# Optimization experiments

Hardware: AMD Instinct MI355X
Metric: run time of the kernel (lower is better)

The kernel has to match this reference:

```python
import jax, jax.numpy as jnp
import numpy as np

B, S, D = 2, 2048, 1024
H, DA, DL = 8, 64, 64   # heads, attention_dim, linear_dim
L = 2                    # num_blocks


def _layernorm(x, w, b, eps):
    mu = jnp.mean(x, axis=-1, keepdims=True)
    var = jnp.mean(jnp.square(x - mu), axis=-1, keepdims=True)
    return (x - mu) * jax.lax.rsqrt(var + eps) * w + b


def _norm_no_affine(x, eps):
    mu = jnp.mean(x, axis=-1, keepdims=True)
    var = jnp.mean(jnp.square(x - mu), axis=-1, keepdims=True)
    return (x - mu) * jax.lax.rsqrt(var + eps)


def setup_inputs() -> dict:
    key = jax.random.key(0)
    ks = jax.random.split(key, 8)
    x = jax.random.normal(ks[0], (B, S, D), dtype=jnp.float32)
    # causal visibility mask: True = visible
    attn_mask = jnp.tril(jnp.ones((S, S), dtype=bool))[None].repeat(B, axis=0)
    proj_dim = DL * 2 * H + DA * 2 * H  # 2048
    uvqk = jax.random.normal(ks[1], (L, D, proj_dim), dtype=jnp.float32) * 0.02
    o_w = jax.random.normal(ks[2], (L, D, DL * H), dtype=jnp.float32) * 0.02  # torch [out,in]
    o_b = jnp.zeros((L, D), dtype=jnp.float32)
    ln_w = jnp.ones((L, D), dtype=jnp.float32)
    ln_b = jnp.zeros((L, D), dtype=jnp.float32)
    last_ln_w = jnp.ones((D,), dtype=jnp.float32)
    last_ln_b = jnp.zeros((D,), dtype=jnp.float32)
    return {"x": x, "attn_mask": attn_mask, "uvqk": uvqk, "o_w": o_w,
            "o_b": o_b, "ln_w": ln_w, "ln_b": ln_b,
            "last_ln_w": last_ln_w, "last_ln_b": last_ln_b}


def reference(x, attn_mask, uvqk, o_w, o_b, ln_w, ln_b, last_ln_w, last_ln_b):
    seq_len = x.shape[1]
    m = attn_mask[:, None, :, :]  # [B,1,S,S]
    for i in range(L):
        h = _layernorm(x, ln_w[i], ln_b[i], 1e-6)                 # [B,S,D]
        proj = jax.nn.silu(jnp.einsum('bsd,de->bse', h, uvqk[i]))  # [B,S,2*(DL+DA)*H]
        u, v, q, k = jnp.split(proj, [DL * H, 2 * DL * H, 2 * DL * H + DA * H], axis=-1)
        q = q.reshape(B, seq_len, H, DA).transpose(0, 2, 1, 3)   # [B,H,S,DA]
        kk = k.reshape(B, seq_len, H, DA).transpose(0, 2, 1, 3)
        vv = v.reshape(B, seq_len, H, DL).transpose(0, 2, 1, 3)  # [B,H,S,DL]
        uu = u.reshape(B, seq_len, H, DL).transpose(0, 2, 1, 3)
        scores = jnp.einsum('bhsd,bhtd->bhst', q, kk)            # [B,H,S,S]
        scores = jnp.where(m, jax.nn.silu(scores) / seq_len, 0.0)
        out = jnp.einsum('bhst,bhtd->bhsd', scores, vv)          # [B,H,S,DL]
        out = _norm_no_affine(out, 1e-6)
        u_dot = (uu * out).transpose(0, 2, 1, 3).reshape(B, seq_len, DL * H)
        x = x + jnp.einsum('bsf,df->bsd', u_dot, o_w[i]) + o_b[i]
    return _layernorm(x, last_ln_w, last_ln_b, 1e-8)
```

## Files before the change

kernel.cpp:

```cpp
#include <hip/hip_runtime.h>

#define B_ 2
#define S_ 2048
#define D_ 1024
#define H_ 8
#define L_ 2
#define P_ 2048
#define F_ 512
#define R_ (B_*S_)

typedef unsigned short u16;
typedef unsigned int u32;
typedef __bf16 bf16;
typedef bf16 bf16x8 __attribute__((ext_vector_type(8)));
typedef short short8 __attribute__((ext_vector_type(8)));
typedef float v4f __attribute__((ext_vector_type(4)));

__device__ __forceinline__ float silu_fast(float x){
  float e = __expf(-x);
  return x * __builtin_amdgcn_rcpf(1.0f + e);
}
__device__ __forceinline__ float bf2f(u16 u){
  union { u32 i; float f; } x; x.i = ((u32)u) << 16; return x.f;
}
__device__ __forceinline__ u16 f2bfu(float f){
  union { float f; u32 i; } x; x.f = f;
  u32 r = x.i + 0x7fff + ((x.i >> 16) & 1);
  return (u16)(r >> 16);
}
__device__ __forceinline__ void gload16(const u16* g, u16* l){
  __builtin_amdgcn_global_load_lds(
      (const __attribute__((address_space(1))) void*)g,
      (__attribute__((address_space(3))) void*)l, 16, 0, 0);
}

__global__ __launch_bounds__(256) void cvt_kernel(const float* __restrict__ x, float* __restrict__ xf){
  int i = (blockIdx.x * 256 + threadIdx.x) * 4;
  *(float4*)(xf + i) = *(const float4*)(x + i);
}

__global__ __launch_bounds__(256) void cvt_bf16_kernel(const float* __restrict__ src, u16* __restrict__ dst){
  int i = (blockIdx.x * 256 + threadIdx.x) * 4;
  float4 v = *(const float4*)(src + i);
  ushort4 o; o.x = f2bfu(v.x); o.y = f2bfu(v.y); o.z = f2bfu(v.z); o.w = f2bfu(v.w);
  *(ushort4*)(dst + i) = o;
}

__global__ __launch_bounds__(256) void cvt_uvqkT_kernel(const float* __restrict__ uvqk, u16* __restrict__ ot){
  __shared__ float t[32][33];
  int l = blockIdx.z;
  int p0 = blockIdx.x * 32, d0 = blockIdx.y * 32;
  int tx = threadIdx.x & 31, ty = threadIdx.x >> 5;
  const float* src = uvqk + ((size_t)l * D_ + d0) * P_ + p0;
  #pragma unroll
  for (int s = 0; s < 4; s++)
    t[ty + s*8][tx] = src[(size_t)(ty + s*8) * P_ + tx];
  __syncthreads();
  u16* dst = ot + ((size_t)l * P_ + p0) * D_ + d0;
  #pragma unroll
  for (int s = 0; s < 4; s++)
    dst[(size_t)(ty + s*8) * D_ + tx] = f2bfu(t[tx][ty + s*8]);
}

__global__ __launch_bounds__(256) void kvpack_kernel(const u16* __restrict__ projh,
    u16* __restrict__ kpack, u16* __restrict__ vpack){
  __shared__ u16 tls[64*72];
  int t = blockIdx.x, t0 = t * 64;
  int bh = blockIdx.y;
  int b = bh >> 3, hh = bh & 7;
  int tid = threadIdx.x;
  const size_t bS = (size_t)b * S_;
  const int voff = F_ + hh*64, koff = 3*F_ + hh*64;
  {
    int row = tid >> 2, c16 = (tid & 3) * 16;
    const u16* sp = projh + (bS + t0 + row) * P_ + voff + c16;
    short8 a = *(const short8*)sp;
    short8 bq = *(const short8*)(sp + 8);
    *(short8*)&tls[row*72 + c16] = a;
    *(short8*)&tls[row*72 + c16 + 8] = bq;
  }
  __syncthreads();
  size_t obase = ((size_t)(bh*32 + t) * 8) * 512;
  #pragma unroll
  for (int pass = 0; pass < 2; pass++){
    int id = tid + pass * 256;
    int c = id >> 6, lane = id & 63;
    int quad = lane >> 4, l15 = lane & 15;
    int cns = c >> 1, ckst = c & 1;
    const u16* kp = projh + (bS + t0 + cns*16 + l15) * P_ + koff + ckst*32 + quad*8;
    *(short8*)(kpack + obase + (size_t)c*512 + lane*8) = *(const short8*)kp;
    short8 vv;
    #pragma unroll
    for (int j = 0; j < 8; j++)
      vv[j] = (short)tls[(ckst*32 + quad*8 + j)*72 + cns*16 + l15];
    *(short8*)(vpack + obase + (size_t)c*512 + lane*8) = vv;
  }
}

__global__ __launch_bounds__(256) void ln_kernel(const float* __restrict__ xf,
    const float* __restrict__ w, const float* __restrict__ b,
    void* __restrict__ outp, float eps, int out_bf16){
  int row = blockIdx.x, tid = threadIdx.x;
  const float* xr = xf + (size_t)row * D_;
  float4 v = *(const float4*)(xr + tid * 4);
  float s  = v.x + v.y + v.z + v.w;
  float sq = v.x*v.x + v.y*v.y + v.z*v.z + v.w*v.w;
  #pragma unroll
  for (int off = 32; off; off >>= 1){ s += __shfl_down(s, off); sq += __shfl_down(sq, off); }
  __shared__ float red[8];
  __shared__ float stats[2];
  int wid = tid >> 6;
  if ((tid & 63) == 0){ red[wid] = s; red[4 + wid] = sq; }
  __syncthreads();
  if (tid == 0){
    float S1 = red[0] + red[1] + red[2] + red[3];
    float S2 = red[4] + red[5] + red[6] + red[7];
    float mu = S1 * (1.0f / D_);
    float var = S2 * (1.0f / D_) - mu * mu;
    stats[0] = mu; stats[1] = rsqrtf(var + eps);
  }
  __syncthreads();
  float mu = stats[0], rs = stats[1];
  int i = tid * 4;
  float4 wv = *(const float4*)(w + i);
  float4 bv = *(const float4*)(b + i);
  float o0 = (v.x - mu) * rs * wv.x + bv.x;
  float o1 = (v.y - mu) * rs * wv.y + bv.y;
  float o2 = (v.z - mu) * rs * wv.z + bv.z;
  float o3 = (v.w - mu) * rs * wv.w + bv.w;
  if (out_bf16){
    ushort4 o; o.x = f2bfu(o0); o.y = f2bfu(o1); o.z = f2bfu(o2); o.w = f2bfu(o3);
    *(ushort4*)((u16*)outp + (size_t)row * D_ + i) = o;
  } else {
    *(float4*)((float*)outp + (size_t)row * D_ + i) = make_float4(o0, o1, o2, o3);
  }
}

template<int KDIM>
__device__ __forceinline__ void gemm_mfma_core(const u16* __restrict__ A,
    const u16* __restrict__ Bt, u16* As, u16* Bs, int m0, int n0, v4f acc[4][4]){
  int tid = threadIdx.x;
  int w = tid >> 6, lane = tid & 63;
  int wm = w >> 1, wn = w & 1, quad = lane >> 4, l15 = lane & 15;
  int srow = lane >> 2, skoct = (lane & 3) * 8;
  for (int kt = 0; kt < KDIM; kt += 32){
    __syncthreads();
    #pragma unroll
    for (int s = 0; s < 2; s++){
      int g = w * 2 + s;
      gload16(A  + (size_t)(m0 + g*16 + srow) * KDIM + kt + skoct, As + g*512);
      gload16(Bt + (size_t)(n0 + g*16 + srow) * KDIM + kt + skoct, Bs + g*512);
    }
    __syncthreads();
    short8 af[4], bfr[4];
    #pragma unroll
    for (int i = 0; i < 4; i++)
      af[i] = *(const short8*)&As[(wm*64 + i*16 + l15)*32 + quad*8];
    #pragma unroll
    for (int j = 0; j < 4; j++)
      bfr[j] = *(const short8*)&Bs[(wn*64 + j*16 + l15)*32 + quad*8];
    #pragma unroll
    for (int i = 0; i < 4; i++)
      #pragma unroll
      for (int j = 0; j < 4; j++)
        acc[i][j] = __builtin_amdgcn_mfma_f32_16x16x32_bf16(
            __builtin_bit_cast(bf16x8, af[i]), __builtin_bit_cast(bf16x8, bfr[j]),
            acc[i][j], 0, 0, 0);
  }
}

__global__ __launch_bounds__(256) void gemm_silu_mfma(const u16* __restrict__ A,
    const u16* __restrict__ Bt, u16* __restrict__ C){
  __shared__ u16 As[128*32], Bs[128*32];
  v4f acc[4][4];
  #pragma unroll
  for (int i = 0; i < 4; i++)
    #pragma unroll
    for (int j = 0; j < 4; j++) acc[i][j] = (v4f){0.f,0.f,0.f,0.f};
  int m0 = blockIdx.y * 128, n0 = blockIdx.x * 128;
  gemm_mfma_core<D_>(A, Bt, As, Bs, m0, n0, acc);
  int tid = threadIdx.x, w = tid >> 6, lane = tid & 63;
  int wm = w >> 1, wn = w & 1, quad = lane >> 4, l15 = lane & 15;
  #pragma unroll
  for (int i = 0; i < 4; i++)
    #pragma unroll
    for (int r = 0; r < 4; r++){
      int m = m0 + wm*64 + i*16 + quad*4 + r;
      u16* cp = C + (size_t)m * P_ + n0 + wn*64 + l15;
      #pragma unroll
      for (int j = 0; j < 4; j++)
        cp[j*16] = f2bfu(silu_fast(acc[i][j][r]));
    }
}

__global__ __launch_bounds__(256) void gemm_add_mfma(const u16* __restrict__ A,
    const u16* __restrict__ Bt, const float* __restrict__ bias, float* __restrict__ X){
  __shared__ u16 As[128*32], Bs[128*32];
  v4f acc[4][4];
  #pragma unroll
  for (int i = 0; i < 4; i++)
    #pragma unroll
    for (int j = 0; j < 4; j++) acc[i][j] = (v4f){0.f,0.f,0.f,0.f};
  int m0 = blockIdx.y * 128, n0 = blockIdx.x * 128;
  gemm_mfma_core<F_>(A, Bt, As, Bs, m0, n0, acc);
  int tid = threadIdx.x, w = tid >> 6, lane = tid & 63;
  int wm = w >> 1, wn = w & 1, quad = lane >> 4, l15 = lane & 15;
  float bj[4];
  #pragma unroll
  for (int j = 0; j < 4; j++) bj[j] = bias[n0 + wn*64 + j*16 + l15];
  #pragma unroll
  for (int i = 0; i < 4; i++)
    #pragma unroll
    for (int r = 0; r < 4; r++){
      int m = m0 + wm*64 + i*16 + quad*4 + r;
      float* xp = X + (size_t)m * D_ + n0 + wn*64 + l15;
      #pragma unroll
      for (int j = 0; j < 4; j++)
        xp[j*16] += acc[i][j][r] + bj[j];
    }
}

__global__ __launch_bounds__(256) void attn_kernel(const u16* __restrict__ projh,
                                                   const u16* __restrict__ kpack,
                                                   const u16* __restrict__ vpack,
                                                   u16* __restrict__ opart){
  __shared__ u16 ks[8*512];
  __shared__ u16 vs[8*512];
  __shared__ u16 Ps[64*72];
  int qt = 15 - (int)blockIdx.x;
  int z  = blockIdx.z;
  int ttop = 2*qt + 1;
  int bh = blockIdx.y;
  int b = bh >> 3, hh = bh & 7;
  int tid = threadIdx.x;
  int w = tid >> 6, lane = tid & 63, quad = lane >> 4, l15 = lane & 15;
  int s0 = qt * 128;
  const size_t bS = (size_t)b * S_;
  const int qoff = 2*F_ + hh*64;

  bf16x8 aq[2][2];
  #pragma unroll
  for (int qh = 0; qh < 2; qh++){
    const u16* qp = projh + (bS + s0 + qh*64 + w*16 + l15) * P_ + qoff + quad*8;
    aq[qh][0] = __builtin_bit_cast(bf16x8, *(const short8*)qp);
    aq[qh][1] = __builtin_bit_cast(bf16x8, *(const short8*)(qp + 32));
  }

  v4f oacc[2][4];
  #pragma unroll
  for (int qh = 0; qh < 2; qh++)
    #pragma unroll
    for (int i = 0; i < 4; i++) oacc[qh][i] = (v4f){0.f, 0.f, 0.f, 0.f};

  for (int t = z; t <= ttop; t += 2){
    size_t pbase = ((size_t)(bh*32 + t) * 8) * 512;
    __syncthreads();
    #pragma unroll
    for (int cc = 0; cc < 2; cc++){
      int c = w + cc*4;
      gload16(kpack + pbase + (size_t)c*512 + lane*8, ks + c*512);
      gload16(vpack + pbase + (size_t)c*512 + lane*8, vs + c*512);
    }
    __syncthreads();

    short8 vf[4][2];
    #pragma unroll
    for (int ds = 0; ds < 4; ds++)
      #pragma unroll
      for (int kst = 0; kst < 2; kst++)
        vf[ds][kst] = *(const short8*)&vs[(ds*2+kst)*512 + lane*8];

    int t0 = t * 64;
    #pragma unroll
    for (int qh = 0; qh < 2; qh++){
      int dtile = 2*qt + qh;
      if (t > dtile) continue;
      v4f sacc[4];
      #pragma unroll
      for (int i = 0; i < 4; i++) sacc[i] = (v4f){0.f, 0.f, 0.f, 0.f};
      #pragma unroll
      for (int ns = 0; ns < 4; ns++){
        bf16x8 bk0 = __builtin_bit_cast(bf16x8, *(const short8*)&ks[(ns*2+0)*512 + lane*8]);
        bf16x8 bk1 = __builtin_bit_cast(bf16x8, *(const short8*)&ks[(ns*2+1)*512 + lane*8]);
        sacc[ns] = __builtin_amdgcn_mfma_f32_16x16x32_bf16(aq[qh][0], bk0, sacc[ns], 0, 0, 0);
        sacc[ns] = __builtin_amdgcn_mfma_f32_16x16x32_bf16(aq[qh][1], bk1, sacc[ns], 0, 0, 0);
      }

      bool diag = (t == dtile);
      #pragma unroll
      for (int ns = 0; ns < 4; ns++){
        #pragma unroll
        for (int r = 0; r < 4; r++){
          int rl = w*16 + quad*4 + r;
          int cl = ns*16 + l15;
          float p = silu_fast(sacc[ns][r]) * (1.0f / S_);
          if (diag && cl > rl) p = 0.0f;
          Ps[rl*72 + cl] = f2bfu(p);
        }
      }
      #pragma unroll
      for (int kst = 0; kst < 2; kst++){
        short8 aps = *(const short8*)&Ps[(w*16 + l15)*72 + kst*32 + quad*8];
        bf16x8 ap = __builtin_bit_cast(bf16x8, aps);
        #pragma unroll
        for (int ds = 0; ds < 4; ds++)
          oacc[qh][ds] = __builtin_amdgcn_mfma_f32_16x16x32_bf16(
              ap, __builtin_bit_cast(bf16x8, vf[ds][kst]), oacc[qh][ds], 0, 0, 0);
      }
    }
  }

  u16* ob = opart + (size_t)z * ((size_t)R_ * F_);
  #pragma unroll
  for (int qh = 0; qh < 2; qh++){
    #pragma unroll
    for (int r = 0; r < 4; r++){
      int sg = s0 + qh*64 + w*16 + quad*4 + r;
      u16* op = ob + (bS + sg) * (size_t)F_ + hh*64 + l15;
      #pragma unroll
      for (int ds = 0; ds < 4; ds++)
        op[ds*16] = f2bfu(oacc[qh][ds][r]);
    }
  }
}

__global__ __launch_bounds__(256) void norm_gate_kernel(const u16* __restrict__ opart,
    const u16* __restrict__ projh, u16* __restrict__ udot){
  int w = threadIdx.x >> 6, lane = threadIdx.x & 63;
  int sg = blockIdx.x * 4 + w;
  int hh = lane >> 3, seg = lane & 7;
  size_t off = (size_t)sg * F_ + hh*64 + seg*8;
  short8 a0 = *(const short8*)(opart + off);
  short8 a1 = *(const short8*)(opart + (size_t)R_ * F_ + off);
  float e[8];
  float s = 0.f, sq = 0.f;
  #pragma unroll
  for (int i = 0; i < 8; i++){
    e[i] = bf2f((u16)a0[i]) + bf2f((u16)a1[i]);
    s += e[i]; sq += e[i]*e[i];
  }
  #pragma unroll
  for (int m = 1; m < 8; m <<= 1){
    s  += __shfl_xor(s, m, 64);
    sq += __shfl_xor(sq, m, 64);
  }
  float mu = s * (1.0f/64.0f);
  float var = sq * (1.0f/64.0f) - mu*mu;
  float rs = rsqrtf(var + 1e-6f);
  const u16* up = projh + (size_t)sg * P_ + hh*64 + seg*8;
  short8 uv = *(const short8*)up;
  short8 ov;
  #pragma unroll
  for (int i = 0; i < 8; i++)
    ov[i] = (short)f2bfu((e[i] - mu) * rs * bf2f((u16)uv[i]));
  *(short8*)(udot + off) = ov;
}

extern "C" void kernel_launch(void* const* d_in, const int* in_sizes, int n_in,
                              void* d_out, int out_size, void* d_ws, size_t ws_size,
                              hipStream_t stream){
  (void)in_sizes; (void)n_in; (void)out_size; (void)ws_size;
  const float* x     = (const float*)d_in[0];
  const float* uvqk  = (const float*)d_in[2];
  const float* o_w   = (const float*)d_in[3];
  const float* o_b   = (const float*)d_in[4];
  const float* ln_w  = (const float*)d_in[5];
  const float* ln_b  = (const float*)d_in[6];
  const float* lln_w = (const float*)d_in[7];
  const float* lln_b = (const float*)d_in[8];
  float* out = (float*)d_out;

  char* ws = (char*)d_ws;
  float* xf    = (float*)ws;
  u16*   h     = (u16*)(ws + (16u<<20));
  u16*   kpack = h;
  u16*   vpack = (u16*)(ws + (20u<<20));
  u16*   udot  = (u16*)(ws + (24u<<20));
  u16*   projh = (u16*)(ws + (28u<<20));
  u16*   uvqkT = (u16*)(ws + (44u<<20));
  u16*   owh   = (u16*)(ws + (52u<<20));
  u16*   opart = (u16*)(ws + (54u<<20));

  cvt_kernel<<<R_ * D_ / 1024, 256, 0, stream>>>(x, xf);
  cvt_uvqkT_kernel<<<dim3(P_/32, D_/32, L_), 256, 0, stream>>>(uvqk, uvqkT);
  cvt_bf16_kernel<<<L_ * D_ * F_ / 1024, 256, 0, stream>>>(o_w, owh);
  for (int l = 0; l < L_; l++){
    ln_kernel<<<R_, 256, 0, stream>>>(xf, ln_w + l * D_, ln_b + l * D_, h, 1e-6f, 1);
    gemm_silu_mfma<<<dim3(P_/128, R_/128), 256, 0, stream>>>(
        h, uvqkT + (size_t)l * P_ * D_, projh);
    kvpack_kernel<<<dim3(S_/64, B_*H_), 256, 0, stream>>>(projh, kpack, vpack);
    attn_kernel<<<dim3(S_/128, B_*H_, 2), 256, 0, stream>>>(projh, kpack, vpack, opart);
    norm_gate_kernel<<<R_/4, 256, 0, stream>>>(opart, projh, udot);
    gemm_add_mfma<<<dim3(D_/128, R_/128), 256, 0, stream>>>(
        udot, owh + (size_t)l * D_ * F_, o_b + l * D_, xf);
  }
  ln_kernel<<<R_, 256, 0, stream>>>(xf, lln_w, lln_b, out, 1e-8f, 0);
}
```

Baseline: 325.6 us.

## Double-buffer LDS tiles in GEMM and attention kernels to overlap loads

Both MFMA GEMM cores and the attention kernel now keep two LDS buffers. The next K-slice or K/V tile is prefetched into the other buffer while MFMAs run on the current one, with a single barrier at the end of each iteration instead of two. The goal is to hide global-to-LDS load latency behind compute. In exchange, LDS use doubles, which may lower occupancy, and correctness relies on the barrier also waiting for the outstanding loads.

```diff
diff --git a/kernel.cpp b/kernel.cpp
--- a/kernel.cpp
+++ b/kernel.cpp
@@ -143,22 +143,28 @@
   int w = tid >> 6, lane = tid & 63;
   int wm = w >> 1, wn = w & 1, quad = lane >> 4, l15 = lane & 15;
   int srow = lane >> 2, skoct = (lane & 3) * 8;
-  for (int kt = 0; kt < KDIM; kt += 32){
-    __syncthreads();
+  auto stage = [&](int buf, int kt){
     #pragma unroll
     for (int s = 0; s < 2; s++){
       int g = w * 2 + s;
-      gload16(A  + (size_t)(m0 + g*16 + srow) * KDIM + kt + skoct, As + g*512);
-      gload16(Bt + (size_t)(n0 + g*16 + srow) * KDIM + kt + skoct, Bs + g*512);
-    }
-    __syncthreads();
+      gload16(A  + (size_t)(m0 + g*16 + srow) * KDIM + kt + skoct, As + buf*4096 + g*512);
+      gload16(Bt + (size_t)(n0 + g*16 + srow) * KDIM + kt + skoct, Bs + buf*4096 + g*512);
+    }
+  };
+  stage(0, 0);
+  __syncthreads();
+  int cur = 0;
+  for (int kt = 0; kt < KDIM; kt += 32){
+    if (kt + 32 < KDIM) stage(cur ^ 1, kt + 32);
+    const u16* asb = As + cur*4096;
+    const u16* bsb = Bs + cur*4096;
     short8 af[4], bfr[4];
     #pragma unroll
     for (int i = 0; i < 4; i++)
-      af[i] = *(const short8*)&As[(wm*64 + i*16 + l15)*32 + quad*8];
+      af[i] = *(const short8*)&asb[(wm*64 + i*16 + l15)*32 + quad*8];
     #pragma unroll
     for (int j = 0; j < 4; j++)
-      bfr[j] = *(const short8*)&Bs[(wn*64 + j*16 + l15)*32 + quad*8];
+      bfr[j] = *(const short8*)&bsb[(wn*64 + j*16 + l15)*32 + quad*8];
     #pragma unroll
     for (int i = 0; i < 4; i++)
       #pragma unroll
@@ -166,12 +172,14 @@
         acc[i][j] = __builtin_amdgcn_mfma_f32_16x16x32_bf16(
             __builtin_bit_cast(bf16x8, af[i]), __builtin_bit_cast(bf16x8, bfr[j]),
             acc[i][j], 0, 0, 0);
+    __syncthreads();
+    cur ^= 1;
   }
 }
 
 __global__ __launch_bounds__(256) void gemm_silu_mfma(const u16* __restrict__ A,
     const u16* __restrict__ Bt, u16* __restrict__ C){
-  __shared__ u16 As[128*32], Bs[128*32];
+  __shared__ u16 As[2*128*32], Bs[2*128*32];
   v4f acc[4][4];
   #pragma unroll
   for (int i = 0; i < 4; i++)
@@ -195,7 +203,7 @@
 
 __global__ __launch_bounds__(256) void gemm_add_mfma(const u16* __restrict__ A,
     const u16* __restrict__ Bt, const float* __restrict__ bias, float* __restrict__ X){
-  __shared__ u16 As[128*32], Bs[128*32];
+  __shared__ u16 As[2*128*32], Bs[2*128*32];
   v4f acc[4][4];
   #pragma unroll
   for (int i = 0; i < 4; i++)
@@ -224,8 +232,8 @@
                                                    const u16* __restrict__ kpack,
                                                    const u16* __restrict__ vpack,
                                                    u16* __restrict__ opart){
-  __shared__ u16 ks[8*512];
-  __shared__ u16 vs[8*512];
+  __shared__ u16 ks[2*8*512];
+  __shared__ u16 vs[2*8*512];
   __shared__ u16 Ps[64*72];
   int qt = 15 - (int)blockIdx.x;
   int z  = blockIdx.z;
@@ -252,25 +260,32 @@
     #pragma unroll
     for (int i = 0; i < 4; i++) oacc[qh][i] = (v4f){0.f, 0.f, 0.f, 0.f};
 
-  for (int t = z; t <= ttop; t += 2){
+  auto stage = [&](int buf, int t){
     size_t pbase = ((size_t)(bh*32 + t) * 8) * 512;
-    __syncthreads();
     #pragma unroll
     for (int cc = 0; cc < 2; cc++){
       int c = w + cc*4;
-      gload16(kpack + pbase + (size_t)c*512 + lane*8, ks + c*512);
-      gload16(vpack + pbase + (size_t)c*512 + lane*8, vs + c*512);
-    }
-    __syncthreads();
+      gload16(kpack + pbase + (size_t)c*512 + lane*8, ks + buf*4096 + c*512);
+      gload16(vpack + pbase + (size_t)c*512 + lane*8, vs + buf*4096 + c*512);
+    }
+  };
+
+  stage(0, z);
+  __syncthreads();
+  int cur = 0;
+
+  for (int t = z; t <= ttop; t += 2){
+    if (t + 2 <= ttop) stage(cur ^ 1, t + 2);
+    const u16* ksb = ks + cur*4096;
+    const u16* vsb = vs + cur*4096;
 
     short8 vf[4][2];
     #pragma unroll
     for (int ds = 0; ds < 4; ds++)
       #pragma unroll
       for (int kst = 0; kst < 2; kst++)
-        vf[ds][kst] = *(const short8*)&vs[(ds*2+kst)*512 + lane*8];
-
-    int t0 = t * 64;
+        vf[ds][kst] = *(const short8*)&vsb[(ds*2+kst)*512 + lane*8];
+
     #pragma unroll
     for (int qh = 0; qh < 2; qh++){
       int dtile = 2*qt + qh;
@@ -280,8 +295,8 @@
       for (int i = 0; i < 4; i++) sacc[i] = (v4f){0.f, 0.f, 0.f, 0.f};
       #pragma unroll
       for (int ns = 0; ns < 4; ns++){
-        bf16x8 bk0 = __builtin_bit_cast(bf16x8, *(const short8*)&ks[(ns*2+0)*512 + lane*8]);
-        bf16x8 bk1 = __builtin_bit_cast(bf16x8, *(const short8*)&ks[(ns*2+1)*512 + lane*8]);
+        bf16x8 bk0 = __builtin_bit_cast(bf16x8, *(const short8*)&ksb[(ns*2+0)*512 + lane*8]);
+        bf16x8 bk1 = __builtin_bit_cast(bf16x8, *(const short8*)&ksb[(ns*2+1)*512 + lane*8]);
         sacc[ns] = __builtin_amdgcn_mfma_f32_16x16x32_bf16(aq[qh][0], bk0, sacc[ns], 0, 0, 0);
         sacc[ns] = __builtin_amdgcn_mfma_f32_16x16x32_bf16(aq[qh][1], bk1, sacc[ns], 0, 0, 0);
       }
@@ -308,6 +323,8 @@
               ap, __builtin_bit_cast(bf16x8, vf[ds][kst]), oacc[qh][ds], 0, 0, 0);
       }
     }
+    __syncthreads();
+    cur ^= 1;
   }
 
   u16* ob = opart + (size_t)z * ((size_t)R_ * F_);
```

New measurement: 333.2 us. 2.4% more time.

## Remap workgroup indices across XCDs and drop initial fp32 copy kernel

Applied to the files above, without the earlier changes.

The GEMM and attention kernels now take a flat 1D grid and permute block indices so that consecutive blocks land on tiles that share data within each XCD (chiplet-aware swizzle). The attention mapping also pairs heavy and light causal query tiles across slots to balance work. The initial x-to-workspace copy kernel is removed: layer 0 reads x directly, and the residual GEMM now reads from a separate input buffer and writes to the output buffer. Risk is in index-mapping correctness and whether the swizzle actually improves L2 locality.

```diff
diff --git a/kernel.cpp b/kernel.cpp
--- a/kernel.cpp
+++ b/kernel.cpp
@@ -32,11 +32,6 @@
   __builtin_amdgcn_global_load_lds(
       (const __attribute__((address_space(1))) void*)g,
       (__attribute__((address_space(3))) void*)l, 16, 0, 0);
-}
-
-__global__ __launch_bounds__(256) void cvt_kernel(const float* __restrict__ x, float* __restrict__ xf){
-  int i = (blockIdx.x * 256 + threadIdx.x) * 4;
-  *(float4*)(xf + i) = *(const float4*)(x + i);
 }
 
 __global__ __launch_bounds__(256) void cvt_bf16_kernel(const float* __restrict__ src, u16* __restrict__ dst){
@@ -97,11 +92,11 @@
   }
 }
 
-__global__ __launch_bounds__(256) void ln_kernel(const float* __restrict__ xf,
+__global__ __launch_bounds__(256) void ln_kernel(const float* __restrict__ src,
     const float* __restrict__ w, const float* __restrict__ b,
     void* __restrict__ outp, float eps, int out_bf16){
   int row = blockIdx.x, tid = threadIdx.x;
-  const float* xr = xf + (size_t)row * D_;
+  const float* xr = src + (size_t)row * D_;
   float4 v = *(const float4*)(xr + tid * 4);
   float s  = v.x + v.y + v.z + v.w;
   float sq = v.x*v.x + v.y*v.y + v.z*v.z + v.w*v.w;
@@ -177,7 +172,10 @@
   for (int i = 0; i < 4; i++)
     #pragma unroll
     for (int j = 0; j < 4; j++) acc[i][j] = (v4f){0.f,0.f,0.f,0.f};
-  int m0 = blockIdx.y * 128, n0 = blockIdx.x * 128;
+  int f = blockIdx.x;
+  int wg = (f & 7) * 64 + (f >> 3);
+  int bx = wg & 15, by = wg >> 4;
+  int m0 = by * 128, n0 = bx * 128;
   gemm_mfma_core<D_>(A, Bt, As, Bs, m0, n0, acc);
   int tid = threadIdx.x, w = tid >> 6, lane = tid & 63;
   int wm = w >> 1, wn = w & 1, quad = lane >> 4, l15 = lane & 15;
@@ -194,14 +192,18 @@
 }
 
 __global__ __launch_bounds__(256) void gemm_add_mfma(const u16* __restrict__ A,
-    const u16* __restrict__ Bt, const float* __restrict__ bias, float* __restrict__ X){
+    const u16* __restrict__ Bt, const float* __restrict__ bias,
+    const float* __restrict__ Xin, float* __restrict__ Xout){
   __shared__ u16 As[128*32], Bs[128*32];
   v4f acc[4][4];
   #pragma unroll
   for (int i = 0; i < 4; i++)
     #pragma unroll
     for (int j = 0; j < 4; j++) acc[i][j] = (v4f){0.f,0.f,0.f,0.f};
-  int m0 = blockIdx.y * 128, n0 = blockIdx.x * 128;
+  int f = blockIdx.x;
+  int wg = (f & 7) * 32 + (f >> 3);
+  int bx = wg & 7, by = wg >> 3;
+  int m0 = by * 128, n0 = bx * 128;
   gemm_mfma_core<F_>(A, Bt, As, Bs, m0, n0, acc);
   int tid = threadIdx.x, w = tid >> 6, lane = tid & 63;
   int wm = w >> 1, wn = w & 1, quad = lane >> 4, l15 = lane & 15;
@@ -213,10 +215,12 @@
     #pragma unroll
     for (int r = 0; r < 4; r++){
       int m = m0 + wm*64 + i*16 + quad*4 + r;
-      float* xp = X + (size_t)m * D_ + n0 + wn*64 + l15;
+      size_t off = (size_t)m * D_ + n0 + wn*64 + l15;
+      const float* xi = Xin + off;
+      float* xo = Xout + off;
       #pragma unroll
       for (int j = 0; j < 4; j++)
-        xp[j*16] += acc[i][j][r] + bj[j];
+        xo[j*16] = xi[j*16] + acc[i][j][r] + bj[j];
     }
 }
 
@@ -227,10 +231,16 @@
   __shared__ u16 ks[8*512];
   __shared__ u16 vs[8*512];
   __shared__ u16 Ps[64*72];
-  int qt = 15 - (int)blockIdx.x;
-  int z  = blockIdx.z;
+  int f = (int)blockIdx.x;
+  int g = f & 7;
+  int s = f >> 3;
+  int c = s & 31;
+  int slot = s >> 5;
+  int z = c >> 4;
+  int x = c & 15;
+  int qt = slot ? x : (15 - x);
+  int bh = g + (slot << 3);
   int ttop = 2*qt + 1;
-  int bh = blockIdx.y;
   int b = bh >> 3, hh = bh & 7;
   int tid = threadIdx.x;
   int w = tid >> 6, lane = tid & 63, quad = lane >> 4, l15 = lane & 15;
@@ -257,9 +267,9 @@
     __syncthreads();
     #pragma unroll
     for (int cc = 0; cc < 2; cc++){
-      int c = w + cc*4;
-      gload16(kpack + pbase + (size_t)c*512 + lane*8, ks + c*512);
-      gload16(vpack + pbase + (size_t)c*512 + lane*8, vs + c*512);
+      int ch = w + cc*4;
+      gload16(kpack + pbase + (size_t)ch*512 + lane*8, ks + ch*512);
+      gload16(vpack + pbase + (size_t)ch*512 + lane*8, vs + ch*512);
     }
     __syncthreads();
 
@@ -270,7 +280,6 @@
       for (int kst = 0; kst < 2; kst++)
         vf[ds][kst] = *(const short8*)&vs[(ds*2+kst)*512 + lane*8];
 
-    int t0 = t * 64;
     #pragma unroll
     for (int qh = 0; qh < 2; qh++){
       int dtile = 2*qt + qh;
@@ -381,18 +390,18 @@
   u16*   owh   = (u16*)(ws + (52u<<20));
   u16*   opart = (u16*)(ws + (54u<<20));
 
-  cvt_kernel<<<R_ * D_ / 1024, 256, 0, stream>>>(x, xf);
   cvt_uvqkT_kernel<<<dim3(P_/32, D_/32, L_), 256, 0, stream>>>(uvqk, uvqkT);
   cvt_bf16_kernel<<<L_ * D_ * F_ / 1024, 256, 0, stream>>>(o_w, owh);
   for (int l = 0; l < L_; l++){
-    ln_kernel<<<R_, 256, 0, stream>>>(xf, ln_w + l * D_, ln_b + l * D_, h, 1e-6f, 1);
-    gemm_silu_mfma<<<dim3(P_/128, R_/128), 256, 0, stream>>>(
+    const float* xsrc = (l == 0) ? x : xf;
+    ln_kernel<<<R_, 256, 0, stream>>>(xsrc, ln_w + l * D_, ln_b + l * D_, h, 1e-6f, 1);
+    gemm_silu_mfma<<<512, 256, 0, stream>>>(
         h, uvqkT + (size_t)l * P_ * D_, projh);
     kvpack_kernel<<<dim3(S_/64, B_*H_), 256, 0, stream>>>(projh, kpack, vpack);
-    attn_kernel<<<dim3(S_/128, B_*H_, 2), 256, 0, stream>>>(projh, kpack, vpack, opart);
+    attn_kernel<<<512, 256, 0, stream>>>(projh, kpack, vpack, opart);
     norm_gate_kernel<<<R_/4, 256, 0, stream>>>(opart, projh, udot);
-    gemm_add_mfma<<<dim3(D_/128, R_/128), 256, 0, stream>>>(
-        udot, owh + (size_t)l * D_ * F_, o_b + l * D_, xf);
+    gemm_add_mfma<<<256, 256, 0, stream>>>(
+        udot, owh + (size_t)l * D_ * F_, o_b + l * D_, xsrc, xf);
   }
   ln_kernel<<<R_, 256, 0, stream>>>(xf, lln_w, lln_b, out, 1e-8f, 0);
 }
```

Measured after the change: 297.1 us. 1.1x faster.
